# Kernel optimization log

Measured on AMD Instinct MI355X. Metric: run time of the kernel, lower is better.

Reference implementation:

```python
import jax, jax.numpy as jnp
import numpy as np

QMAX = 127.0  # 8-bit narrow-range symmetric: values in [-127, 127]


def _quantize_per_tensor(t):
    """Symmetric per-tensor int8 quantization (narrow range, like Brevitas Int8*PerTensorFloat).
    Returns (int8 codes as int32 for matmul, float scale)."""
    scale = jnp.max(jnp.abs(t)) / QMAX
    q = jnp.clip(jnp.round(t / scale), -QMAX, QMAX).astype(jnp.int8)
    return q, scale


def setup_inputs() -> dict:
    key = jax.random.key(0)
    k_x, k_w, k_b = jax.random.split(key, 3)
    size_in, size_out, n = 1024, 1024, 32768
    x = jax.random.normal(k_x, (n, size_in), dtype=jnp.float32)
    # kaiming_uniform_(a=sqrt(5)) on [size_out, size_in] -> bound = 1/sqrt(size_in)
    bound = 1.0 / np.sqrt(size_in)
    weight = jax.random.uniform(k_w, (size_out, size_in), dtype=jnp.float32,
                                minval=-bound, maxval=bound)
    bias = jax.random.uniform(k_b, (size_out,), dtype=jnp.float32,
                              minval=-bound, maxval=bound)
    return {"x": x, "weight": weight, "bias": bias}


def reference(x, weight, bias):
    # Quantize activations and weights to int8 per-tensor symmetric.
    qx, sx = _quantize_per_tensor(x)        # [N, K] int8, scalar scale
    qw, sw = _quantize_per_tensor(weight)   # [M, K] int8, scalar scale
    # Approximate-multiplier GEMM modeled as exact int8 MAC with int32 accum
    # (mul8s_acc is the accurate 8-bit multiplier LUT).
    acc = jnp.matmul(qx.astype(jnp.int32), qw.astype(jnp.int32).T)  # [N, M] int32
    # Rescale: output / ((QMAX/input_scale) * (QMAX/weight_scale)) with
    # Brevitas scale conventions == acc * sx * sw here.
    out = acc.astype(jnp.float32) * (sx * sw)
    return out + bias
```

## Files before the change

kernel.cpp:

```cpp
#include <hip/hip_runtime.h>
#include <cstdint>
#include <cstddef>


typedef int v4i __attribute__((ext_vector_type(4)));

#define QMAXF 127.0f
#define KDIM 1024
#define MDIM 1024

__global__ void init_ws(unsigned* amax) {
  amax[0] = 0u;
  amax[1] = 0u;
}

__global__ void absmax2(const float4* __restrict__ x, int nx4,
                        const float4* __restrict__ w, int nw4,
                        unsigned* __restrict__ amax) {
  const float4* p = (blockIdx.y == 0) ? x : w;
  int n4 = (blockIdx.y == 0) ? nx4 : nw4;
  float m = 0.0f;
  for (int i = blockIdx.x * blockDim.x + threadIdx.x; i < n4;
       i += gridDim.x * blockDim.x) {
    float4 v = p[i];
    m = fmaxf(m, fmaxf(fmaxf(fabsf(v.x), fabsf(v.y)),
                       fmaxf(fabsf(v.z), fabsf(v.w))));
  }
  for (int off = 32; off; off >>= 1) m = fmaxf(m, __shfl_down(m, off, 64));
  __shared__ float wm[4];
  int lane = threadIdx.x & 63, wid = threadIdx.x >> 6;
  if (lane == 0) wm[wid] = m;
  __syncthreads();
  if (threadIdx.x == 0) {
    float bm = wm[0];
    for (int i = 1; i < ((int)blockDim.x >> 6); ++i) bm = fmaxf(bm, wm[i]);
    atomicMax(&amax[blockIdx.y], __float_as_uint(bm));
  }
}

__global__ void quant2(const float4* __restrict__ x, int nx4,
                       const float4* __restrict__ w, int nw4,
                       const unsigned* __restrict__ amax,
                       int* __restrict__ qx, int* __restrict__ qw) {
  int sel = blockIdx.y;
  const float4* p = sel ? w : x;
  int n4 = sel ? nw4 : nx4;
  int* q = sel ? qw : qx;
  float s = __uint_as_float(amax[sel]) / QMAXF;
  for (int i = blockIdx.x * blockDim.x + threadIdx.x; i < n4;
       i += gridDim.x * blockDim.x) {
    float4 v = p[i];
    int b0 = (int)fminf(fmaxf(rintf(v.x / s), -QMAXF), QMAXF);
    int b1 = (int)fminf(fmaxf(rintf(v.y / s), -QMAXF), QMAXF);
    int b2 = (int)fminf(fmaxf(rintf(v.z / s), -QMAXF), QMAXF);
    int b3 = (int)fminf(fmaxf(rintf(v.w / s), -QMAXF), QMAXF);
    unsigned packed = ((unsigned)(b0 & 255)) | ((unsigned)(b1 & 255) << 8) |
                      ((unsigned)(b2 & 255) << 16) | ((unsigned)(b3 & 255) << 24);
    q[i] = (int)packed;
  }
}

__device__ __forceinline__ void ld_lds16(const void* g, void* l) {
  __builtin_amdgcn_global_load_lds(
      (__attribute__((address_space(1))) void*)(void*)g,
      (__attribute__((address_space(3))) void*)l, 16, 0, 0);
}

__global__ __launch_bounds__(256) void gemm_i8(
    const char* __restrict__ qx, const char* __restrict__ qw,
    const float* __restrict__ bias, const unsigned* __restrict__ amax,
    float* __restrict__ out) {
  __shared__ __align__(16) char smA[128 * 64];
  __shared__ __align__(16) char smB[128 * 64];

  const int tid = threadIdx.x;
  const int wave = tid >> 6;
  const int lane = tid & 63;
  const int bm = blockIdx.x;
  const int bn = blockIdx.y;
  const int wn = wave >> 1;
  const int wm = wave & 1;

  const char* xbase = qx + (size_t)(bn * 128) * KDIM;
  const char* wbase = qw + (size_t)(bm * 128) * KDIM;

  v4i acc[4][4] = {};

  const int srow = wave * 32 + (lane >> 2);
  const int skb = (lane & 3) * 16;

  for (int kt = 0; kt < KDIM / 64; ++kt) {
    const int kb = kt * 64;
    ld_lds16(xbase + (size_t)srow * KDIM + kb + skb, smA + (wave * 32) * 64);
    ld_lds16(xbase + (size_t)(srow + 16) * KDIM + kb + skb,
             smA + (wave * 32 + 16) * 64);
    ld_lds16(wbase + (size_t)srow * KDIM + kb + skb, smB + (wave * 32) * 64);
    ld_lds16(wbase + (size_t)(srow + 16) * KDIM + kb + skb,
             smB + (wave * 32 + 16) * 64);
    __syncthreads();

    const int kq = (lane >> 4) * 16;
    v4i afrag[4], bfrag[4];
#pragma unroll
    for (int i = 0; i < 4; ++i)
      afrag[i] = *(const v4i*)(smA + (wn * 64 + i * 16 + (lane & 15)) * 64 + kq);
#pragma unroll
    for (int j = 0; j < 4; ++j)
      bfrag[j] = *(const v4i*)(smB + (wm * 64 + j * 16 + (lane & 15)) * 64 + kq);

#pragma unroll
    for (int i = 0; i < 4; ++i)
#pragma unroll
      for (int j = 0; j < 4; ++j)
        acc[i][j] =
            __builtin_amdgcn_mfma_i32_16x16x64_i8(afrag[i], bfrag[j], acc[i][j], 0, 0, 0);
    __syncthreads();
  }

  const float s = (__uint_as_float(amax[0]) / QMAXF) *
                  (__uint_as_float(amax[1]) / QMAXF);
  const int mcol = bm * 128 + wm * 64 + (lane & 15);
  const int nbase = bn * 128 + wn * 64 + ((lane >> 4) << 2);
  float bv[4];
#pragma unroll
  for (int j = 0; j < 4; ++j) bv[j] = bias[mcol + j * 16];
#pragma unroll
  for (int i = 0; i < 4; ++i) {
#pragma unroll
    for (int r = 0; r < 4; ++r) {
      const int n = nbase + i * 16 + r;
      float* orow = out + (size_t)n * MDIM + mcol;
#pragma unroll
      for (int j = 0; j < 4; ++j)
        orow[j * 16] = (float)acc[i][j][r] * s + bv[j];
    }
  }
}

extern "C" void kernel_launch(void* const* d_in, const int* in_sizes, int n_in,
                              void* d_out, int out_size, void* d_ws, size_t ws_size,
                              hipStream_t stream) {
  const float* x = (const float*)d_in[0];
  const float* w = (const float*)d_in[1];
  const float* bias = (const float*)d_in[2];
  float* out = (float*)d_out;

  const int NX = in_sizes[0];
  const int NW = in_sizes[1];
  const int N = NX / KDIM;

  unsigned* amax = (unsigned*)d_ws;
  char* qx = (char*)d_ws + 64;
  char* qw = qx + (size_t)NX;

  init_ws<<<1, 1, 0, stream>>>(amax);

  dim3 rgrid(1024, 2);
  absmax2<<<rgrid, 256, 0, stream>>>((const float4*)x, NX / 4,
                                     (const float4*)w, NW / 4, amax);

  quant2<<<rgrid, 256, 0, stream>>>((const float4*)x, NX / 4,
                                    (const float4*)w, NW / 4, amax,
                                    (int*)qx, (int*)qw);

  dim3 ggrid(MDIM / 128, N / 128);
  gemm_i8<<<ggrid, 256, 0, stream>>>(qx, qw, bias, amax, out);
}
```

Baseline: 313.3 us.

## Drop atomic absmax init kernel, widen quant stores, use K=128 swizzled LDS tiles

Replaces the init plus atomicMax absmax reduction with per-block partial maxima that each quant block re-reduces, which removes one kernel launch and the atomics. The quant kernel now multiplies by a reciprocal instead of dividing and writes 16 bytes per thread. The GEMM stages 128-wide K tiles with an XOR swizzle, halving the number of barrier rounds and avoiding LDS bank conflicts. Multiplying by the reciprocal can round differently from true division in rare edge cases.

```diff
diff --git a/kernel.cpp b/kernel.cpp
--- a/kernel.cpp
+++ b/kernel.cpp
@@ -8,55 +8,96 @@
 #define QMAXF 127.0f
 #define KDIM 1024
 #define MDIM 1024
-
-__global__ void init_ws(unsigned* amax) {
-  amax[0] = 0u;
-  amax[1] = 0u;
-}
-
-__global__ void absmax2(const float4* __restrict__ x, int nx4,
-                        const float4* __restrict__ w, int nw4,
-                        unsigned* __restrict__ amax) {
-  const float4* p = (blockIdx.y == 0) ? x : w;
-  int n4 = (blockIdx.y == 0) ? nx4 : nw4;
-  float m = 0.0f;
-  for (int i = blockIdx.x * blockDim.x + threadIdx.x; i < n4;
-       i += gridDim.x * blockDim.x) {
+#define NBX 512
+#define NBW 32
+
+__global__ __launch_bounds__(256) void absmax_partial(
+    const float4* __restrict__ x, int nx4,
+    const float4* __restrict__ w, int nw4,
+    float* __restrict__ partials) {
+  const int b = blockIdx.x;
+  const bool isw = (b >= NBX);
+  const float4* __restrict__ p = isw ? w : x;
+  const int n4 = isw ? nw4 : nx4;
+  const int nb = isw ? NBW : NBX;
+  const int bb = isw ? (b - NBX) : b;
+  const int stride = nb * 256;
+
+  float m0 = 0.f, m1 = 0.f, m2 = 0.f, m3 = 0.f;
+  int i = bb * 256 + threadIdx.x;
+  for (; i + 3 * stride < n4; i += 4 * stride) {
+    float4 v0 = p[i], v1 = p[i + stride], v2 = p[i + 2 * stride],
+           v3 = p[i + 3 * stride];
+    m0 = fmaxf(m0, fmaxf(fmaxf(fabsf(v0.x), fabsf(v0.y)),
+                         fmaxf(fabsf(v0.z), fabsf(v0.w))));
+    m1 = fmaxf(m1, fmaxf(fmaxf(fabsf(v1.x), fabsf(v1.y)),
+                         fmaxf(fabsf(v1.z), fabsf(v1.w))));
+    m2 = fmaxf(m2, fmaxf(fmaxf(fabsf(v2.x), fabsf(v2.y)),
+                         fmaxf(fabsf(v2.z), fabsf(v2.w))));
+    m3 = fmaxf(m3, fmaxf(fmaxf(fabsf(v3.x), fabsf(v3.y)),
+                         fmaxf(fabsf(v3.z), fabsf(v3.w))));
+  }
+  for (; i < n4; i += stride) {
     float4 v = p[i];
-    m = fmaxf(m, fmaxf(fmaxf(fabsf(v.x), fabsf(v.y)),
-                       fmaxf(fabsf(v.z), fabsf(v.w))));
-  }
+    m0 = fmaxf(m0, fmaxf(fmaxf(fabsf(v.x), fabsf(v.y)),
+                         fmaxf(fabsf(v.z), fabsf(v.w))));
+  }
+  float m = fmaxf(fmaxf(m0, m1), fmaxf(m2, m3));
   for (int off = 32; off; off >>= 1) m = fmaxf(m, __shfl_down(m, off, 64));
   __shared__ float wm[4];
-  int lane = threadIdx.x & 63, wid = threadIdx.x >> 6;
+  const int lane = threadIdx.x & 63, wid = threadIdx.x >> 6;
+  if (lane == 0) wm[wid] = m;
+  __syncthreads();
+  if (threadIdx.x == 0)
+    partials[b] = fmaxf(fmaxf(wm[0], wm[1]), fmaxf(wm[2], wm[3]));
+}
+
+__global__ __launch_bounds__(256) void quant2(
+    const float4* __restrict__ x, int nx16,
+    const float4* __restrict__ w, int nw16,
+    const float* __restrict__ partials,
+    v4i* __restrict__ qx, v4i* __restrict__ qw,
+    float* __restrict__ amax_out) {
+  const int sel = blockIdx.y;
+  const float* pp = partials + (sel ? NBX : 0);
+  const int np = sel ? NBW : NBX;
+  float m = 0.f;
+  for (int i = threadIdx.x; i < np; i += 256) m = fmaxf(m, pp[i]);
+  for (int off = 32; off; off >>= 1) m = fmaxf(m, __shfl_down(m, off, 64));
+  __shared__ float wm[4];
+  __shared__ float bmax;
+  const int lane = threadIdx.x & 63, wid = threadIdx.x >> 6;
   if (lane == 0) wm[wid] = m;
   __syncthreads();
   if (threadIdx.x == 0) {
-    float bm = wm[0];
-    for (int i = 1; i < ((int)blockDim.x >> 6); ++i) bm = fmaxf(bm, wm[i]);
-    atomicMax(&amax[blockIdx.y], __float_as_uint(bm));
-  }
-}
-
-__global__ void quant2(const float4* __restrict__ x, int nx4,
-                       const float4* __restrict__ w, int nw4,
-                       const unsigned* __restrict__ amax,
-                       int* __restrict__ qx, int* __restrict__ qw) {
-  int sel = blockIdx.y;
-  const float4* p = sel ? w : x;
-  int n4 = sel ? nw4 : nx4;
-  int* q = sel ? qw : qx;
-  float s = __uint_as_float(amax[sel]) / QMAXF;
-  for (int i = blockIdx.x * blockDim.x + threadIdx.x; i < n4;
-       i += gridDim.x * blockDim.x) {
-    float4 v = p[i];
-    int b0 = (int)fminf(fmaxf(rintf(v.x / s), -QMAXF), QMAXF);
-    int b1 = (int)fminf(fmaxf(rintf(v.y / s), -QMAXF), QMAXF);
-    int b2 = (int)fminf(fmaxf(rintf(v.z / s), -QMAXF), QMAXF);
-    int b3 = (int)fminf(fmaxf(rintf(v.w / s), -QMAXF), QMAXF);
-    unsigned packed = ((unsigned)(b0 & 255)) | ((unsigned)(b1 & 255) << 8) |
-                      ((unsigned)(b2 & 255) << 16) | ((unsigned)(b3 & 255) << 24);
-    q[i] = (int)packed;
+    float bm = fmaxf(fmaxf(wm[0], wm[1]), fmaxf(wm[2], wm[3]));
+    bmax = bm;
+    if (blockIdx.x == 0) amax_out[sel] = bm;
+  }
+  __syncthreads();
+  const float amax = bmax;
+  const float r = QMAXF / amax;
+
+  const float4* __restrict__ p = sel ? w : x;
+  const int n16 = sel ? nw16 : nx16;
+  v4i* __restrict__ q = sel ? qw : qx;
+
+  for (int i = blockIdx.x * 256 + threadIdx.x; i < n16;
+       i += gridDim.x * 256) {
+    float4 v0 = p[4 * i], v1 = p[4 * i + 1], v2 = p[4 * i + 2],
+           v3 = p[4 * i + 3];
+    v4i o;
+#define QPK(V)                                                         \
+  ((((int)fminf(fmaxf(rintf((V).x * r), -QMAXF), QMAXF)) & 255) |      \
+   ((((int)fminf(fmaxf(rintf((V).y * r), -QMAXF), QMAXF)) & 255) << 8) | \
+   ((((int)fminf(fmaxf(rintf((V).z * r), -QMAXF), QMAXF)) & 255) << 16) | \
+   ((((int)fminf(fmaxf(rintf((V).w * r), -QMAXF), QMAXF)) & 255) << 24))
+    o[0] = QPK(v0);
+    o[1] = QPK(v1);
+    o[2] = QPK(v2);
+    o[3] = QPK(v3);
+#undef QPK
+    q[i] = o;
   }
 }
 
@@ -68,10 +109,10 @@
 
 __global__ __launch_bounds__(256) void gemm_i8(
     const char* __restrict__ qx, const char* __restrict__ qw,
-    const float* __restrict__ bias, const unsigned* __restrict__ amax,
+    const float* __restrict__ bias, const float* __restrict__ amax,
     float* __restrict__ out) {
-  __shared__ __align__(16) char smA[128 * 64];
-  __shared__ __align__(16) char smB[128 * 64];
+  __shared__ __align__(16) char smA[128 * 128];
+  __shared__ __align__(16) char smB[128 * 128];
 
   const int tid = threadIdx.x;
   const int wave = tid >> 6;
@@ -81,44 +122,51 @@
   const int wn = wave >> 1;
   const int wm = wave & 1;
 
-  const char* xbase = qx + (size_t)(bn * 128) * KDIM;
-  const char* wbase = qw + (size_t)(bm * 128) * KDIM;
+  const char* xb = qx + (size_t)(bn * 128) * KDIM;
+  const char* wb = qw + (size_t)(bm * 128) * KDIM;
 
   v4i acc[4][4] = {};
 
-  const int srow = wave * 32 + (lane >> 2);
-  const int skb = (lane & 3) * 16;
-
-  for (int kt = 0; kt < KDIM / 64; ++kt) {
-    const int kb = kt * 64;
-    ld_lds16(xbase + (size_t)srow * KDIM + kb + skb, smA + (wave * 32) * 64);
-    ld_lds16(xbase + (size_t)(srow + 16) * KDIM + kb + skb,
-             smA + (wave * 32 + 16) * 64);
-    ld_lds16(wbase + (size_t)srow * KDIM + kb + skb, smB + (wave * 32) * 64);
-    ld_lds16(wbase + (size_t)(srow + 16) * KDIM + kb + skb,
-             smB + (wave * 32 + 16) * 64);
+  const int lrow = lane >> 3;
+  const int sgx = (lane & 7) ^ lrow;
+
+  for (int kt = 0; kt < 8; ++kt) {
+    const int kb = kt * 128;
+#pragma unroll
+    for (int c = 0; c < 4; ++c) {
+      const int rbase = c * 32 + wave * 8;
+      ld_lds16(xb + (size_t)(rbase + lrow) * KDIM + kb + sgx * 16,
+               smA + rbase * 128);
+      ld_lds16(wb + (size_t)(rbase + lrow) * KDIM + kb + sgx * 16,
+               smB + rbase * 128);
+    }
     __syncthreads();
 
-    const int kq = (lane >> 4) * 16;
-    v4i afrag[4], bfrag[4];
-#pragma unroll
-    for (int i = 0; i < 4; ++i)
-      afrag[i] = *(const v4i*)(smA + (wn * 64 + i * 16 + (lane & 15)) * 64 + kq);
-#pragma unroll
-    for (int j = 0; j < 4; ++j)
-      bfrag[j] = *(const v4i*)(smB + (wm * 64 + j * 16 + (lane & 15)) * 64 + kq);
-
-#pragma unroll
-    for (int i = 0; i < 4; ++i)
-#pragma unroll
-      for (int j = 0; j < 4; ++j)
-        acc[i][j] =
-            __builtin_amdgcn_mfma_i32_16x16x64_i8(afrag[i], bfrag[j], acc[i][j], 0, 0, 0);
+#pragma unroll
+    for (int kc = 0; kc < 2; ++kc) {
+      const int s = kc * 4 + (lane >> 4);
+      v4i a[4], b[4];
+#pragma unroll
+      for (int i = 0; i < 4; ++i) {
+        const int r = wn * 64 + i * 16 + (lane & 15);
+        a[i] = *(const v4i*)(smA + r * 128 + ((s ^ (r & 7)) * 16));
+      }
+#pragma unroll
+      for (int j = 0; j < 4; ++j) {
+        const int r = wm * 64 + j * 16 + (lane & 15);
+        b[j] = *(const v4i*)(smB + r * 128 + ((s ^ (r & 7)) * 16));
+      }
+#pragma unroll
+      for (int i = 0; i < 4; ++i)
+#pragma unroll
+        for (int j = 0; j < 4; ++j)
+          acc[i][j] = __builtin_amdgcn_mfma_i32_16x16x64_i8(a[i], b[j],
+                                                            acc[i][j], 0, 0, 0);
+    }
     __syncthreads();
   }
 
-  const float s = (__uint_as_float(amax[0]) / QMAXF) *
-                  (__uint_as_float(amax[1]) / QMAXF);
+  const float s = (amax[0] / QMAXF) * (amax[1] / QMAXF);
   const int mcol = bm * 128 + wm * 64 + (lane & 15);
   const int nbase = bn * 128 + wn * 64 + ((lane >> 4) << 2);
   float bv[4];
@@ -149,19 +197,18 @@
   const int NW = in_sizes[1];
   const int N = NX / KDIM;
 
-  unsigned* amax = (unsigned*)d_ws;
-  char* qx = (char*)d_ws + 64;
+  float* amax = (float*)d_ws;
+  float* partials = (float*)((char*)d_ws + 64);
+  char* qx = (char*)d_ws + 4096;
   char* qw = qx + (size_t)NX;
 
-  init_ws<<<1, 1, 0, stream>>>(amax);
-
-  dim3 rgrid(1024, 2);
-  absmax2<<<rgrid, 256, 0, stream>>>((const float4*)x, NX / 4,
-                                     (const float4*)w, NW / 4, amax);
-
-  quant2<<<rgrid, 256, 0, stream>>>((const float4*)x, NX / 4,
-                                    (const float4*)w, NW / 4, amax,
-                                    (int*)qx, (int*)qw);
+  absmax_partial<<<NBX + NBW, 256, 0, stream>>>(
+      (const float4*)x, NX / 4, (const float4*)w, NW / 4, partials);
+
+  dim3 qgrid(1024, 2);
+  quant2<<<qgrid, 256, 0, stream>>>((const float4*)x, NX / 16,
+                                    (const float4*)w, NW / 16, partials,
+                                    (v4i*)qx, (v4i*)qw, amax);
 
   dim3 ggrid(MDIM / 128, N / 128);
   gemm_i8<<<ggrid, 256, 0, stream>>>(qx, qw, bias, amax, out);
```

Result: faster. 298.1 us (-4.8%).
